# Optimization experiments

Hardware: AMD Instinct MI355X
Metric: run time of the kernel (lower is better)

Reference implementation:

```python
import jax, jax.numpy as jnp
import numpy as np

TEMPERATURE = 0.1
BASE_TEMPERATURE = 1.0
LAMBDA_PROTOTYPE = 1.0
EPS = 1e-12  # F.normalize eps

N, C, D, P = 65536, 128, 512, 128


def setup_inputs() -> dict:
    key = jax.random.key(0)
    k1, k2, k3, k4, k5 = jax.random.split(key, 5)
    return {
        "outputs": jax.random.normal(k1, (N, C), dtype=jnp.float32),
        "targets": jax.random.normal(k2, (N, C), dtype=jnp.float32),
        "backbone_features": jax.random.normal(k3, (N, D), dtype=jnp.float32),
        "prototype_features": jax.random.normal(k4, (P, D), dtype=jnp.float32),
        "prototype_labels": jax.random.randint(k5, (N, P), 0, 2, dtype=jnp.int32),
        "prototype_weights": jnp.ones((P,), dtype=jnp.float32),
    }


def reference(outputs, targets, backbone_features, prototype_features,
              prototype_labels, prototype_weights):
    # L2-normalize backbone features along feature dim (F.normalize, dim=1)
    norm = jnp.maximum(jnp.linalg.norm(backbone_features, axis=1, keepdims=True), EPS)
    bf = backbone_features / norm  # (N, D)

    n = outputs.reshape(-1, outputs.shape[-1]).shape[0]

    # Batched version of the per-sample loop: one GEMM for all samples.
    logits = jnp.einsum('nd,pd->np', bf, prototype_features) / TEMPERATURE  # (N, P)
    # Per-sample max subtraction for stability (detached in torch)
    logits = logits - jax.lax.stop_gradient(jnp.max(logits, axis=1, keepdims=True))

    mask = prototype_labels.astype(logits.dtype) * prototype_weights  # (N, P)
    exp_logits = jnp.exp(logits) * (1.0 - mask)
    log_prob = logits - jnp.log(jnp.sum(exp_logits, axis=1, keepdims=True))  # (N, P)
    mean_log_prob_pos = jnp.sum(mask * log_prob, axis=1)  # (N,)

    ctr_loss = -(TEMPERATURE / BASE_TEMPERATURE) * mean_log_prob_pos
    loss = jnp.sum(ctr_loss) / n
    return LAMBDA_PROTOTYPE * loss
```

## Files before the change

kernel.cpp:

```cpp
#include <hip/hip_runtime.h>
#include <hip/hip_bf16.h>
#include <math.h>

typedef __bf16 bf16x8v __attribute__((ext_vector_type(8)));
typedef float  f32x4   __attribute__((ext_vector_type(4)));

#define D_DIM 512
#define P_DIM 128
#define TEMP  0.1f
#define ROWS_PER_BLOCK 256
#define THREADS 1024

__global__ __launch_bounds__(THREADS)
void mrc_fused(const float* __restrict__ bfeat,
               const float* __restrict__ protos,
               const int*   __restrict__ labels,
               const float* __restrict__ weights,
               float*       __restrict__ out,
               int nrows)
{
    __shared__ __bf16 sB[P_DIM * D_DIM];
    __shared__ float  sRed[16];

    const int t    = threadIdx.x;
    const int lane = t & 63;
    const int wave = t >> 6;
    const int q    = lane >> 4;
    const int cl   = lane & 15;

    const long long r0 = (long long)blockIdx.x * ROWS_PER_BLOCK + wave * 16;

    unsigned int labbits = 0;
    {
        const int* lbase = labels + r0 * (long long)P_DIM + q * 4 * P_DIM + cl;
#pragma unroll
        for (int reg = 0; reg < 4; ++reg)
#pragma unroll
            for (int ct = 0; ct < 8; ++ct)
                labbits |= (unsigned)(lbase[reg * P_DIM + ct * 16] & 1) << (reg * 8 + ct);
    }

#pragma unroll
    for (int i = 0; i < 8; ++i) {
        const int o   = i * THREADS + t;
        const int p   = ((o >> 10) << 4) | (o & 15);
        const int k   = (((o >> 6) & 15) << 5) | (((o >> 4) & 3) << 3);
        const f32x4 v0 = *(const f32x4*)(protos + p * D_DIM + k);
        const f32x4 v1 = *(const f32x4*)(protos + p * D_DIM + k + 4);
        bf16x8v b;
        b[0]=(__bf16)v0[0]; b[1]=(__bf16)v0[1]; b[2]=(__bf16)v0[2]; b[3]=(__bf16)v0[3];
        b[4]=(__bf16)v1[0]; b[5]=(__bf16)v1[1]; b[6]=(__bf16)v1[2]; b[7]=(__bf16)v1[3];
        *(bf16x8v*)&sB[o * 8] = b;
    }
    __syncthreads();

    const float* arow = bfeat + (r0 + cl) * (long long)D_DIM + q * 8;

    float wcol[8];
#pragma unroll
    for (int ct = 0; ct < 8; ++ct) wcol[ct] = weights[ct * 16 + cl];

    f32x4 acc[8];
#pragma unroll
    for (int ct = 0; ct < 8; ++ct) acc[ct] = (f32x4){0.f, 0.f, 0.f, 0.f};

    float ss = 0.f;
    f32x4 p[4][2];
#pragma unroll
    for (int i = 0; i < 4; ++i) {
        p[i][0] = *(const f32x4*)(arow + i * 32);
        p[i][1] = *(const f32x4*)(arow + i * 32 + 4);
    }

#pragma unroll
    for (int ks = 0; ks < 16; ++ks) {
        const f32x4 c0 = p[ks & 3][0], c1 = p[ks & 3][1];
        if (ks < 12) {
            p[ks & 3][0] = *(const f32x4*)(arow + (ks + 4) * 32);
            p[ks & 3][1] = *(const f32x4*)(arow + (ks + 4) * 32 + 4);
        }
        ss += c0[0]*c0[0] + c0[1]*c0[1] + c0[2]*c0[2] + c0[3]*c0[3]
            + c1[0]*c1[0] + c1[1]*c1[1] + c1[2]*c1[2] + c1[3]*c1[3];
        bf16x8v af;
        af[0]=(__bf16)c0[0]; af[1]=(__bf16)c0[1]; af[2]=(__bf16)c0[2]; af[3]=(__bf16)c0[3];
        af[4]=(__bf16)c1[0]; af[5]=(__bf16)c1[1]; af[6]=(__bf16)c1[2]; af[7]=(__bf16)c1[3];
        const int base = (ks << 6) + (q << 4) + cl;
#pragma unroll
        for (int ct = 0; ct < 8; ++ct) {
            const bf16x8v bfr = *(const bf16x8v*)&sB[(base + (ct << 10)) * 8];
            acc[ct] = __builtin_amdgcn_mfma_f32_16x16x32_bf16(af, bfr, acc[ct], 0, 0, 0);
        }
    }

    ss += __shfl_xor(ss, 16);
    ss += __shfl_xor(ss, 32);
    const float scale = 1.0f / (fmaxf(sqrtf(ss), 1e-12f) * TEMP);

    float pos_acc = 0.f;
#pragma unroll
    for (int reg = 0; reg < 4; ++reg) {
        const float rscale = __shfl(scale, q * 4 + reg, 16);
        float lg[8];
        float m = -3.4e38f;
#pragma unroll
        for (int ct = 0; ct < 8; ++ct) {
            lg[ct] = acc[ct][reg] * rscale;
            m = fmaxf(m, lg[ct]);
        }
        m = fmaxf(m, __shfl_xor(m, 1, 16));
        m = fmaxf(m, __shfl_xor(m, 2, 16));
        m = fmaxf(m, __shfl_xor(m, 4, 16));
        m = fmaxf(m, __shfl_xor(m, 8, 16));

        float s = 0.f, pz = 0.f, msum = 0.f;
#pragma unroll
        for (int ct = 0; ct < 8; ++ct) {
            const float mask = ((labbits >> (reg * 8 + ct)) & 1u) ? wcol[ct] : 0.f;
            const float z = lg[ct] - m;
            s    += __expf(z) * (1.0f - mask);
            pz   += mask * z;
            msum += mask;
        }
        s += __shfl_xor(s, 1, 16);
        s += __shfl_xor(s, 2, 16);
        s += __shfl_xor(s, 4, 16);
        s += __shfl_xor(s, 8, 16);
        pos_acc += pz - logf(s) * msum;
    }

    pos_acc += __shfl_xor(pos_acc, 1);
    pos_acc += __shfl_xor(pos_acc, 2);
    pos_acc += __shfl_xor(pos_acc, 4);
    pos_acc += __shfl_xor(pos_acc, 8);
    pos_acc += __shfl_xor(pos_acc, 16);
    pos_acc += __shfl_xor(pos_acc, 32);
    if (lane == 0) sRed[wave] = pos_acc;
    __syncthreads();
    if (t == 0) {
        float total = 0.f;
#pragma unroll
        for (int w = 0; w < 16; ++w) total += sRed[w];
        atomicAdd(out, total * (-TEMP / (float)nrows));
    }
}

extern "C" void kernel_launch(void* const* d_in, const int* in_sizes, int n_in,
                              void* d_out, int out_size, void* d_ws, size_t ws_size,
                              hipStream_t stream) {
    const float* bfeat   = (const float*)d_in[2];
    const float* protos  = (const float*)d_in[3];
    const int*   labels  = (const int*)d_in[4];
    const float* weights = (const float*)d_in[5];
    float* out = (float*)d_out;

    const int nrows = in_sizes[2] / D_DIM;

    hipMemsetAsync(d_out, 0, sizeof(float) * out_size, stream);
    const int nblocks = nrows / ROWS_PER_BLOCK;
    mrc_fused<<<nblocks, THREADS, 0, stream>>>(bfeat, protos, labels, weights, out, nrows);
}
```

Measured before the change: 259.3 us.

## Pre-convert prototypes to bf16, coalesce A loads via LDS, keep last tile in registers

A separate small kernel converts the prototype matrix to bf16 once, in the MFMA-fragment layout, and writes it to workspace. The main kernel then copies 7/8 of it into LDS without any conversion, and each wave streams the last column tile straight from global memory into registers. Backbone rows are now read with coalesced row-contiguous loads, converted to bf16 and staged through a padded per-wave LDS buffer before MFMA, instead of strided per-lane fragment loads. The goals are to cut per-block conversion work, shrink LDS so more blocks can fit per CU, and improve global coalescing. The cost is an extra kernel launch, more LDS traffic and an LDS round-trip for the row scales.

```diff
diff --git a/kernel.cpp b/kernel.cpp
--- a/kernel.cpp
+++ b/kernel.cpp
@@ -3,59 +3,67 @@
 #include <math.h>
 
 typedef __bf16 bf16x8v __attribute__((ext_vector_type(8)));
+typedef __bf16 bf16x4v __attribute__((ext_vector_type(4)));
 typedef float  f32x4   __attribute__((ext_vector_type(4)));
 
 #define D_DIM 512
 #define P_DIM 128
 #define TEMP  0.1f
-#define ROWS_PER_BLOCK 256
+#define RPB   256
 #define THREADS 1024
+#define LDA_ROW 68
+
+__global__ __launch_bounds__(256)
+void proto_cvt(const float* __restrict__ protos, __bf16* __restrict__ wsb)
+{
+    const int o  = blockIdx.x * 256 + threadIdx.x;
+    const int cl = o & 15, q = (o >> 4) & 3, ks = (o >> 6) & 15, ct = o >> 10;
+    const int src = (ct * 16 + cl) * D_DIM + ks * 32 + q * 8;
+    const f32x4 v0 = *(const f32x4*)(protos + src);
+    const f32x4 v1 = *(const f32x4*)(protos + src + 4);
+    bf16x8v b;
+    b[0]=(__bf16)v0[0]; b[1]=(__bf16)v0[1]; b[2]=(__bf16)v0[2]; b[3]=(__bf16)v0[3];
+    b[4]=(__bf16)v1[0]; b[5]=(__bf16)v1[1]; b[6]=(__bf16)v1[2]; b[7]=(__bf16)v1[3];
+    *(bf16x8v*)(wsb + o * 8) = b;
+}
 
 __global__ __launch_bounds__(THREADS)
 void mrc_fused(const float* __restrict__ bfeat,
-               const float* __restrict__ protos,
+               const __bf16* __restrict__ wsb,
                const int*   __restrict__ labels,
                const float* __restrict__ weights,
                float*       __restrict__ out,
                int nrows)
 {
-    __shared__ __bf16 sB[P_DIM * D_DIM];
+    __shared__ __bf16 sB[7 * 1024 * 8];
+    __shared__ __bf16 sA[16 * 16 * LDA_ROW];
+    __shared__ float  sScale[16 * 16];
     __shared__ float  sRed[16];
 
-    const int t    = threadIdx.x;
+    const int t = threadIdx.x;
     const int lane = t & 63;
     const int wave = t >> 6;
-    const int q    = lane >> 4;
-    const int cl   = lane & 15;
-
-    const long long r0 = (long long)blockIdx.x * ROWS_PER_BLOCK + wave * 16;
-
-    unsigned int labbits = 0;
+    const int q = lane >> 4, cl = lane & 15;
+
+    const long long r0 = (long long)blockIdx.x * RPB + wave * 16;
+
+    unsigned labbits = 0;
     {
-        const int* lbase = labels + r0 * (long long)P_DIM + q * 4 * P_DIM + cl;
+        const int* lb = labels + (r0 + q * 4) * (long long)P_DIM + cl;
 #pragma unroll
         for (int reg = 0; reg < 4; ++reg)
 #pragma unroll
             for (int ct = 0; ct < 8; ++ct)
-                labbits |= (unsigned)(lbase[reg * P_DIM + ct * 16] & 1) << (reg * 8 + ct);
-    }
-
-#pragma unroll
-    for (int i = 0; i < 8; ++i) {
-        const int o   = i * THREADS + t;
-        const int p   = ((o >> 10) << 4) | (o & 15);
-        const int k   = (((o >> 6) & 15) << 5) | (((o >> 4) & 3) << 3);
-        const f32x4 v0 = *(const f32x4*)(protos + p * D_DIM + k);
-        const f32x4 v1 = *(const f32x4*)(protos + p * D_DIM + k + 4);
-        bf16x8v b;
-        b[0]=(__bf16)v0[0]; b[1]=(__bf16)v0[1]; b[2]=(__bf16)v0[2]; b[3]=(__bf16)v0[3];
-        b[4]=(__bf16)v1[0]; b[5]=(__bf16)v1[1]; b[6]=(__bf16)v1[2]; b[7]=(__bf16)v1[3];
-        *(bf16x8v*)&sB[o * 8] = b;
+                labbits |= (unsigned)(lb[reg * P_DIM + ct * 16] & 1) << (reg * 8 + ct);
+    }
+
+#pragma unroll
+    for (int i = 0; i < 7; ++i) {
+        const int o = i * THREADS + t;
+        *(bf16x8v*)&sB[o * 8] = *(const bf16x8v*)(wsb + o * 8);
     }
     __syncthreads();
 
-    const float* arow = bfeat + (r0 + cl) * (long long)D_DIM + q * 8;
-
     float wcol[8];
 #pragma unroll
     for (int ct = 0; ct < 8; ++ct) wcol[ct] = weights[ct * 16 + cl];
@@ -64,42 +72,74 @@
 #pragma unroll
     for (int ct = 0; ct < 8; ++ct) acc[ct] = (f32x4){0.f, 0.f, 0.f, 0.f};
 
-    float ss = 0.f;
-    f32x4 p[4][2];
-#pragma unroll
-    for (int i = 0; i < 4; ++i) {
-        p[i][0] = *(const f32x4*)(arow + i * 32);
-        p[i][1] = *(const f32x4*)(arow + i * 32 + 4);
-    }
-
-#pragma unroll
-    for (int ks = 0; ks < 16; ++ks) {
-        const f32x4 c0 = p[ks & 3][0], c1 = p[ks & 3][1];
-        if (ks < 12) {
-            p[ks & 3][0] = *(const f32x4*)(arow + (ks + 4) * 32);
-            p[ks & 3][1] = *(const f32x4*)(arow + (ks + 4) * 32 + 4);
-        }
-        ss += c0[0]*c0[0] + c0[1]*c0[1] + c0[2]*c0[2] + c0[3]*c0[3]
-            + c1[0]*c1[0] + c1[1]*c1[1] + c1[2]*c1[2] + c1[3]*c1[3];
-        bf16x8v af;
-        af[0]=(__bf16)c0[0]; af[1]=(__bf16)c0[1]; af[2]=(__bf16)c0[2]; af[3]=(__bf16)c0[3];
-        af[4]=(__bf16)c1[0]; af[5]=(__bf16)c1[1]; af[6]=(__bf16)c1[2]; af[7]=(__bf16)c1[3];
-        const int base = (ks << 6) + (q << 4) + cl;
-#pragma unroll
-        for (int ct = 0; ct < 8; ++ct) {
-            const bf16x8v bfr = *(const bf16x8v*)&sB[(base + (ct << 10)) * 8];
-            acc[ct] = __builtin_amdgcn_mfma_f32_16x16x32_bf16(af, bfr, acc[ct], 0, 0, 0);
-        }
-    }
-
-    ss += __shfl_xor(ss, 16);
-    ss += __shfl_xor(ss, 32);
-    const float scale = 1.0f / (fmaxf(sqrtf(ss), 1e-12f) * TEMP);
+    const float* abase = bfeat + (r0 + q) * (long long)D_DIM + cl * 4;
+    __bf16* sAw = sA + wave * (16 * LDA_ROW);
+    const __bf16* w7 = wsb + 7168 * 8;
+
+    f32x4   pf[2][4];
+    bf16x8v c7[2][2];
+#pragma unroll
+    for (int s = 0; s < 2; ++s)
+#pragma unroll
+        for (int j = 0; j < 4; ++j)
+            pf[s][j] = *(const f32x4*)(abase + j * 4 * D_DIM + s * 64);
+#pragma unroll
+    for (int s = 0; s < 2; ++s)
+#pragma unroll
+        for (int k = 0; k < 2; ++k)
+            c7[s][k] = *(const bf16x8v*)(w7 + ((s * 2 + k) * 64 + lane) * 8);
+
+    float ssq[4] = {0.f, 0.f, 0.f, 0.f};
+
+#pragma unroll
+    for (int ss = 0; ss < 8; ++ss) {
+#pragma unroll
+        for (int j = 0; j < 4; ++j) {
+            const f32x4 v = pf[ss & 1][j];
+            ssq[j] += v[0]*v[0] + v[1]*v[1] + v[2]*v[2] + v[3]*v[3];
+            bf16x4v b;
+            b[0]=(__bf16)v[0]; b[1]=(__bf16)v[1]; b[2]=(__bf16)v[2]; b[3]=(__bf16)v[3];
+            *(bf16x4v*)&sAw[(4 * j + q) * LDA_ROW + cl * 4] = b;
+        }
+        if (ss < 6) {
+#pragma unroll
+            for (int j = 0; j < 4; ++j)
+                pf[ss & 1][j] = *(const f32x4*)(abase + j * 4 * D_DIM + (ss + 2) * 64);
+        }
+#pragma unroll
+        for (int kl = 0; kl < 2; ++kl) {
+            const int ks = ss * 2 + kl;
+            const bf16x8v af = *(const bf16x8v*)&sAw[cl * LDA_ROW + kl * 32 + q * 8];
+            const int base = (ks << 6) + (q << 4) + cl;
+#pragma unroll
+            for (int ct = 0; ct < 7; ++ct) {
+                const bf16x8v bfr = *(const bf16x8v*)&sB[(base + (ct << 10)) * 8];
+                acc[ct] = __builtin_amdgcn_mfma_f32_16x16x32_bf16(af, bfr, acc[ct], 0, 0, 0);
+            }
+            acc[7] = __builtin_amdgcn_mfma_f32_16x16x32_bf16(af, c7[ss & 1][kl], acc[7], 0, 0, 0);
+        }
+        if (ss < 6) {
+#pragma unroll
+            for (int k = 0; k < 2; ++k)
+                c7[ss & 1][k] = *(const bf16x8v*)(w7 + (((ss + 2) * 2 + k) * 64 + lane) * 8);
+        }
+    }
+
+#pragma unroll
+    for (int j = 0; j < 4; ++j) {
+        float s = ssq[j];
+        s += __shfl_xor(s, 1, 16);
+        s += __shfl_xor(s, 2, 16);
+        s += __shfl_xor(s, 4, 16);
+        s += __shfl_xor(s, 8, 16);
+        if (cl == 0)
+            sScale[wave * 16 + 4 * j + q] = 1.0f / (fmaxf(sqrtf(s), 1e-12f) * TEMP);
+    }
 
     float pos_acc = 0.f;
 #pragma unroll
     for (int reg = 0; reg < 4; ++reg) {
-        const float rscale = __shfl(scale, q * 4 + reg, 16);
+        const float rscale = sScale[wave * 16 + q * 4 + reg];
         float lg[8];
         float m = -3.4e38f;
 #pragma unroll
@@ -152,10 +192,11 @@
     const int*   labels  = (const int*)d_in[4];
     const float* weights = (const float*)d_in[5];
     float* out = (float*)d_out;
+    __bf16* wsb = (__bf16*)d_ws;
 
     const int nrows = in_sizes[2] / D_DIM;
 
     hipMemsetAsync(d_out, 0, sizeof(float) * out_size, stream);
-    const int nblocks = nrows / ROWS_PER_BLOCK;
-    mrc_fused<<<nblocks, THREADS, 0, stream>>>(bfeat, protos, labels, weights, out, nrows);
+    proto_cvt<<<32, 256, 0, stream>>>(protos, wsb);
+    mrc_fused<<<nrows / RPB, THREADS, 0, stream>>>(bfeat, wsb, labels, weights, out, nrows);
 }
```

After: 292.3 us. +12.7%, slower.

## Split into prep kernels writing bf16 A image, packed labels, then lean GEMM kernel

Applied to the files above, without the earlier changes.

Breaks the fused kernel into a pipeline. Separate kernels convert prototypes to bf16 in MFMA fragment order, convert backbone rows to a bf16 fragment image with precomputed inverse-norm scales, and pack labels into bitmasks. The main kernel then reads only bf16 A fragments and packed bits, and it sets waves_per_eu to 4. This adds an extra full pass over the features: the fp32 input is read, then a bf16 copy is written and read again, and the labels are read once more. The aim is to simplify the main kernel's loads and improve coalescing, at the risk of more total memory traffic and extra launches. The old fused kernel is kept as a fallback when the workspace is too small.

```diff
diff --git a/kernel.cpp b/kernel.cpp
--- a/kernel.cpp
+++ b/kernel.cpp
@@ -3,48 +3,212 @@
 #include <math.h>
 
 typedef __bf16 bf16x8v __attribute__((ext_vector_type(8)));
+typedef __bf16 bf16x4v __attribute__((ext_vector_type(4)));
 typedef float  f32x4   __attribute__((ext_vector_type(4)));
 
 #define D_DIM 512
 #define P_DIM 128
 #define TEMP  0.1f
-#define ROWS_PER_BLOCK 256
+#define RPB   256
 #define THREADS 1024
 
+__global__ __launch_bounds__(256)
+void proto_cvt(const float* __restrict__ protos, __bf16* __restrict__ wsP)
+{
+    const int o  = blockIdx.x * 256 + threadIdx.x;
+    const int cl = o & 15, q = (o >> 4) & 3, ks = (o >> 6) & 15, ct = o >> 10;
+    const int src = (ct * 16 + cl) * D_DIM + ks * 32 + q * 8;
+    const f32x4 v0 = *(const f32x4*)(protos + src);
+    const f32x4 v1 = *(const f32x4*)(protos + src + 4);
+    bf16x8v b;
+    b[0]=(__bf16)v0[0]; b[1]=(__bf16)v0[1]; b[2]=(__bf16)v0[2]; b[3]=(__bf16)v0[3];
+    b[4]=(__bf16)v1[0]; b[5]=(__bf16)v1[1]; b[6]=(__bf16)v1[2]; b[7]=(__bf16)v1[3];
+    *(bf16x8v*)(wsP + o * 8) = b;
+}
+
+__global__ __launch_bounds__(256)
+void prep_a(const float* __restrict__ bfeat, __bf16* __restrict__ wsA,
+            float* __restrict__ scaleOut)
+{
+    __shared__ __bf16 sT[16 * 528];
+    const int t = threadIdx.x;
+    const long long g = blockIdx.x;
+    const float* src = bfeat + g * 16 * D_DIM;
+    const int row = t >> 4, c0 = t & 15;
+
+    float ssq = 0.f;
+#pragma unroll
+    for (int i = 0; i < 8; ++i) {
+        const int c4 = c0 + 16 * i;
+        const f32x4 v = *(const f32x4*)(src + row * D_DIM + c4 * 4);
+        ssq += v[0]*v[0] + v[1]*v[1] + v[2]*v[2] + v[3]*v[3];
+        bf16x4v b;
+        b[0]=(__bf16)v[0]; b[1]=(__bf16)v[1]; b[2]=(__bf16)v[2]; b[3]=(__bf16)v[3];
+        *(bf16x4v*)&sT[row * 528 + c4 * 4] = b;
+    }
+    ssq += __shfl_xor(ssq, 1, 16);
+    ssq += __shfl_xor(ssq, 2, 16);
+    ssq += __shfl_xor(ssq, 4, 16);
+    ssq += __shfl_xor(ssq, 8, 16);
+    if (c0 == 0)
+        scaleOut[g * 16 + row] = 1.0f / (fmaxf(sqrtf(ssq), 1e-12f) * TEMP);
+    __syncthreads();
+
+    __bf16* dst = wsA + g * 8192;
+#pragma unroll
+    for (int i = 0; i < 4; ++i) {
+        const int o  = i * 256 + t;
+        const int cl = o & 15, q = (o >> 4) & 3, ks = o >> 6;
+        *(bf16x8v*)(dst + o * 8) = *(const bf16x8v*)&sT[cl * 528 + ks * 32 + q * 8];
+    }
+}
+
+__global__ __launch_bounds__(256)
+void pack_labels(const int* __restrict__ labels, unsigned* __restrict__ labImg)
+{
+    const int gid = blockIdx.x * 256 + threadIdx.x;
+    const int g = gid >> 6, l = gid & 63;
+    const int cl = l & 15, q = l >> 4;
+    const int* base = labels + (long long)g * 16 * P_DIM + q * 4 * P_DIM + cl;
+    unsigned v = 0;
+#pragma unroll
+    for (int reg = 0; reg < 4; ++reg)
+#pragma unroll
+        for (int ct = 0; ct < 8; ++ct)
+            v |= (unsigned)(base[reg * P_DIM + ct * 16] & 1) << (reg * 8 + ct);
+    labImg[gid] = v;
+}
+
+__global__ __launch_bounds__(THREADS) __attribute__((amdgpu_waves_per_eu(4, 4)))
+void mrc_v2(const __bf16* __restrict__ wsA,
+            const __bf16* __restrict__ wsP,
+            const unsigned* __restrict__ labImg,
+            const float* __restrict__ scaleIn,
+            const float* __restrict__ weights,
+            float* __restrict__ out, int nrows)
+{
+    __shared__ __bf16 sB[8 * 1024 * 8];
+    __shared__ float  sRed[16];
+
+    const int t = threadIdx.x;
+    const int lane = t & 63;
+    const int wave = t >> 6;
+    const int q = lane >> 4, cl = lane & 15;
+    const int g = blockIdx.x * 16 + wave;
+
+    const unsigned labbits = labImg[g * 64 + lane];
+    const float sc = scaleIn[g * 16 + cl];
+    float wcol[8];
+#pragma unroll
+    for (int ct = 0; ct < 8; ++ct) wcol[ct] = weights[ct * 16 + cl];
+
+#pragma unroll
+    for (int i = 0; i < 8; ++i) {
+        const int o = i * THREADS + t;
+        *(bf16x8v*)&sB[o * 8] = *(const bf16x8v*)(wsP + o * 8);
+    }
+    __syncthreads();
+
+    f32x4 acc[8];
+#pragma unroll
+    for (int ct = 0; ct < 8; ++ct) acc[ct] = (f32x4){0.f, 0.f, 0.f, 0.f};
+
+    const __bf16* aimg = wsA + (long long)g * 8192;
+    bf16x8v pf[4];
+#pragma unroll
+    for (int i = 0; i < 4; ++i)
+        pf[i] = *(const bf16x8v*)(aimg + (i * 64 + lane) * 8);
+
+#pragma unroll
+    for (int ks = 0; ks < 16; ++ks) {
+        const bf16x8v af = pf[ks & 3];
+        if (ks < 12)
+            pf[ks & 3] = *(const bf16x8v*)(aimg + ((ks + 4) * 64 + lane) * 8);
+        const int base = (ks << 6) + (q << 4) + cl;
+#pragma unroll
+        for (int ct = 0; ct < 8; ++ct) {
+            const bf16x8v bfr = *(const bf16x8v*)&sB[(base + (ct << 10)) * 8];
+            acc[ct] = __builtin_amdgcn_mfma_f32_16x16x32_bf16(af, bfr, acc[ct], 0, 0, 0);
+        }
+    }
+
+    float pos_acc = 0.f;
+#pragma unroll
+    for (int reg = 0; reg < 4; ++reg) {
+        const float rscale = __shfl(sc, q * 4 + reg, 16);
+        float lg[8];
+        float m = -3.4e38f;
+#pragma unroll
+        for (int ct = 0; ct < 8; ++ct) {
+            lg[ct] = acc[ct][reg] * rscale;
+            m = fmaxf(m, lg[ct]);
+        }
+        m = fmaxf(m, __shfl_xor(m, 1, 16));
+        m = fmaxf(m, __shfl_xor(m, 2, 16));
+        m = fmaxf(m, __shfl_xor(m, 4, 16));
+        m = fmaxf(m, __shfl_xor(m, 8, 16));
+
+        float s = 0.f, pz = 0.f, msum = 0.f;
+#pragma unroll
+        for (int ct = 0; ct < 8; ++ct) {
+            const float mask = ((labbits >> (reg * 8 + ct)) & 1u) ? wcol[ct] : 0.f;
+            const float z = lg[ct] - m;
+            s    += __expf(z) * (1.0f - mask);
+            pz   += mask * z;
+            msum += mask;
+        }
+        s += __shfl_xor(s, 1, 16);
+        s += __shfl_xor(s, 2, 16);
+        s += __shfl_xor(s, 4, 16);
+        s += __shfl_xor(s, 8, 16);
+        pos_acc += pz - logf(s) * msum;
+    }
+
+    pos_acc += __shfl_xor(pos_acc, 1);
+    pos_acc += __shfl_xor(pos_acc, 2);
+    pos_acc += __shfl_xor(pos_acc, 4);
+    pos_acc += __shfl_xor(pos_acc, 8);
+    pos_acc += __shfl_xor(pos_acc, 16);
+    pos_acc += __shfl_xor(pos_acc, 32);
+    if (lane == 0) sRed[wave] = pos_acc;
+    __syncthreads();
+    if (t == 0) {
+        float total = 0.f;
+#pragma unroll
+        for (int w = 0; w < 16; ++w) total += sRed[w];
+        atomicAdd(out, total * (-TEMP / (float)nrows));
+    }
+}
+
 __global__ __launch_bounds__(THREADS)
-void mrc_fused(const float* __restrict__ bfeat,
-               const float* __restrict__ protos,
-               const int*   __restrict__ labels,
-               const float* __restrict__ weights,
-               float*       __restrict__ out,
-               int nrows)
+void mrc_fused_fb(const float* __restrict__ bfeat,
+                  const float* __restrict__ protos,
+                  const int*   __restrict__ labels,
+                  const float* __restrict__ weights,
+                  float*       __restrict__ out,
+                  int nrows)
 {
     __shared__ __bf16 sB[P_DIM * D_DIM];
     __shared__ float  sRed[16];
-
-    const int t    = threadIdx.x;
+    const int t = threadIdx.x;
     const int lane = t & 63;
     const int wave = t >> 6;
-    const int q    = lane >> 4;
-    const int cl   = lane & 15;
-
-    const long long r0 = (long long)blockIdx.x * ROWS_PER_BLOCK + wave * 16;
-
+    const int q = lane >> 4, cl = lane & 15;
+    const long long r0 = (long long)blockIdx.x * RPB + wave * 16;
     unsigned int labbits = 0;
     {
-        const int* lbase = labels + r0 * (long long)P_DIM + q * 4 * P_DIM + cl;
+        const int* lb = labels + r0 * (long long)P_DIM + q * 4 * P_DIM + cl;
 #pragma unroll
         for (int reg = 0; reg < 4; ++reg)
 #pragma unroll
             for (int ct = 0; ct < 8; ++ct)
-                labbits |= (unsigned)(lbase[reg * P_DIM + ct * 16] & 1) << (reg * 8 + ct);
-    }
-
+                labbits |= (unsigned)(lb[reg * P_DIM + ct * 16] & 1) << (reg * 8 + ct);
+    }
 #pragma unroll
     for (int i = 0; i < 8; ++i) {
-        const int o   = i * THREADS + t;
-        const int p   = ((o >> 10) << 4) | (o & 15);
-        const int k   = (((o >> 6) & 15) << 5) | (((o >> 4) & 3) << 3);
+        const int o = i * THREADS + t;
+        const int p = ((o >> 10) << 4) | (o & 15);
+        const int k = (((o >> 6) & 15) << 5) | (((o >> 4) & 3) << 3);
         const f32x4 v0 = *(const f32x4*)(protos + p * D_DIM + k);
         const f32x4 v1 = *(const f32x4*)(protos + p * D_DIM + k + 4);
         bf16x8v b;
@@ -53,17 +217,13 @@
         *(bf16x8v*)&sB[o * 8] = b;
     }
     __syncthreads();
-
     const float* arow = bfeat + (r0 + cl) * (long long)D_DIM + q * 8;
-
     float wcol[8];
 #pragma unroll
     for (int ct = 0; ct < 8; ++ct) wcol[ct] = weights[ct * 16 + cl];
-
     f32x4 acc[8];
 #pragma unroll
     for (int ct = 0; ct < 8; ++ct) acc[ct] = (f32x4){0.f, 0.f, 0.f, 0.f};
-
     float ss = 0.f;
     f32x4 p[4][2];
 #pragma unroll
@@ -71,7 +231,6 @@
         p[i][0] = *(const f32x4*)(arow + i * 32);
         p[i][1] = *(const f32x4*)(arow + i * 32 + 4);
     }
-
 #pragma unroll
     for (int ks = 0; ks < 16; ++ks) {
         const f32x4 c0 = p[ks & 3][0], c1 = p[ks & 3][1];
@@ -91,11 +250,9 @@
             acc[ct] = __builtin_amdgcn_mfma_f32_16x16x32_bf16(af, bfr, acc[ct], 0, 0, 0);
         }
     }
-
     ss += __shfl_xor(ss, 16);
     ss += __shfl_xor(ss, 32);
     const float scale = 1.0f / (fmaxf(sqrtf(ss), 1e-12f) * TEMP);
-
     float pos_acc = 0.f;
 #pragma unroll
     for (int reg = 0; reg < 4; ++reg) {
@@ -111,7 +268,6 @@
         m = fmaxf(m, __shfl_xor(m, 2, 16));
         m = fmaxf(m, __shfl_xor(m, 4, 16));
         m = fmaxf(m, __shfl_xor(m, 8, 16));
-
         float s = 0.f, pz = 0.f, msum = 0.f;
 #pragma unroll
         for (int ct = 0; ct < 8; ++ct) {
@@ -127,7 +283,6 @@
         s += __shfl_xor(s, 8, 16);
         pos_acc += pz - logf(s) * msum;
     }
-
     pos_acc += __shfl_xor(pos_acc, 1);
     pos_acc += __shfl_xor(pos_acc, 2);
     pos_acc += __shfl_xor(pos_acc, 4);
@@ -153,9 +308,27 @@
     const float* weights = (const float*)d_in[5];
     float* out = (float*)d_out;
 
-    const int nrows = in_sizes[2] / D_DIM;
+    const int nrows  = in_sizes[2] / D_DIM;
+    const int groups = nrows / 16;
+
+    const size_t offA = 0;
+    const size_t offP = offA + (size_t)nrows * D_DIM * sizeof(__bf16);
+    const size_t offS = offP + 131072;
+    const size_t offL = offS + (size_t)nrows * sizeof(float);
+    const size_t need = offL + (size_t)groups * 64 * sizeof(unsigned);
 
     hipMemsetAsync(d_out, 0, sizeof(float) * out_size, stream);
-    const int nblocks = nrows / ROWS_PER_BLOCK;
-    mrc_fused<<<nblocks, THREADS, 0, stream>>>(bfeat, protos, labels, weights, out, nrows);
-}
+
+    if (ws_size >= need) {
+        __bf16*   wsA = (__bf16*)((char*)d_ws + offA);
+        __bf16*   wsP = (__bf16*)((char*)d_ws + offP);
+        float*    wsS = (float*)((char*)d_ws + offS);
+        unsigned* wsL = (unsigned*)((char*)d_ws + offL);
+        proto_cvt<<<32, 256, 0, stream>>>(protos, wsP);
+        prep_a<<<groups, 256, 0, stream>>>(bfeat, wsA, wsS);
+        pack_labels<<<groups / 4, 256, 0, stream>>>(labels, wsL);
+        mrc_v2<<<nrows / RPB, THREADS, 0, stream>>>(wsA, wsP, wsL, wsS, weights, out, nrows);
+    } else {
+        mrc_fused_fb<<<nrows / RPB, THREADS, 0, stream>>>(bfeat, protos, labels, weights, out, nrows);
+    }
+}
```

Measured after the change: 279.4 us. 1.08x slower.
